# Optimization experiments

Hardware: AMD Instinct MI355X
Metric: run time of the kernel (lower is better)

## Reference

```python
import jax, jax.numpy as jnp
import numpy as np

N_HEAD = 16
EPS = 1e-5


def setup_inputs() -> dict:
    key = jax.random.key(0)
    ks = jax.random.split(key, 9)
    B, T, C = 2, 1024, 1024
    s = 0.02
    return {
        "x": jax.random.normal(ks[0], (B, T, C), jnp.float32),
        "Wq": jax.random.normal(ks[1], (C, C), jnp.float32) * s,
        "Wk": jax.random.normal(ks[2], (C, C), jnp.float32) * s,
        "Wv": jax.random.normal(ks[3], (C, C), jnp.float32) * s,
        "Wq2": jax.random.normal(ks[4], (C, C), jnp.float32) * s,
        "Wk2": jax.random.normal(ks[5], (C, C), jnp.float32) * s,
        "Wo": jax.random.normal(ks[6], (C, C), jnp.float32) * s,
        "mixture": jnp.full((1,), -5.0, jnp.float32),  # quartet_gate_init
        "quartet_scale": jnp.ones((1,), jnp.float32),
    }


def reference(x, Wq, Wk, Wv, Wq2, Wk2, Wo, mixture, quartet_scale):
    B, T, C = x.shape
    H = N_HEAD
    Dh = C // H
    scale = 1.0 / jnp.sqrt(jnp.asarray(Dh, x.dtype))

    def heads(W):
        # torch Linear: y = x @ W.T ; then view(B,T,H,Dh).transpose(1,2)
        return (x @ W.T).reshape(B, T, H, Dh).transpose(0, 2, 1, 3)  # [B,H,T,Dh]

    q, k, v = heads(Wq), heads(Wk), heads(Wv)
    q2, k2 = heads(Wq2), heads(Wk2)

    qk = jnp.einsum("bhqd,bhkd->bhqk", q, k) * scale      # [B,H,T,T]
    q2k2 = jnp.einsum("bhqd,bhkd->bhqk", q2, k2) * scale  # [B,H,T,T]

    def row_norm(s):
        mu = s.mean(axis=-1, keepdims=True)
        sigma = s.std(axis=-1, keepdims=True, ddof=1)  # torch std is unbiased
        return (s - mu) / (sigma + EPS)

    qk_n = row_norm(qk)
    q2k2_n = row_norm(q2k2)
    m = jax.nn.sigmoid(mixture)  # [1], broadcasts
    scores = (1.0 - m) * qk_n + m * (qk_n * q2k2_n) * quartet_scale

    causal = jnp.tril(jnp.ones((T, T), bool))  # [T,T]
    scores = jnp.where(causal, scores, -jnp.inf)
    attn = jax.nn.softmax(scores, axis=-1)  # [B,H,T,T]

    y = jnp.einsum("bhqk,bhkd->bhqd", attn, v)  # [B,H,T,Dh]
    y = y.transpose(0, 2, 1, 3).reshape(B, T, C)
    return y @ Wo.T
```

## Files before the change

kernel.cpp:

```cpp
#include <hip/hip_runtime.h>
#include <hip/hip_bf16.h>
#include <stdint.h>

#define TS 1024
#define CS 1024
#define NH 16
#define DHEAD 64
#define NBATCH 2
#define EPSV 1e-5f
#define MEG 1048576

typedef __bf16 bf16x8 __attribute__((ext_vector_type(8)));
typedef float  f32x4  __attribute__((ext_vector_type(4)));

#define MFMA(a, b, c) __builtin_amdgcn_mfma_f32_16x16x32_bf16((a), (b), (c), 0, 0, 0)

__device__ __forceinline__ float bf2f(ushort u){
  union { uint32_t i; float f; } v; v.i = ((uint32_t)u) << 16; return v.f;
}
__device__ __forceinline__ ushort f2bf(float f){
  union { float f; uint32_t i; } v; v.f = f;
  uint32_t r = v.i + 0x7FFFu + ((v.i >> 16) & 1u);
  return (ushort)(r >> 16);
}

__device__ __forceinline__ void gl_lds16(const ushort* g, ushort* l) {
  __builtin_amdgcn_global_load_lds(
      (const __attribute__((address_space(1))) void*)g,
      (__attribute__((address_space(3))) void*)l, 16, 0, 0);
}

__global__ __launch_bounds__(256)
void cast_all(const float* __restrict__ x,
              const float* __restrict__ Wq, const float* __restrict__ Wk,
              const float* __restrict__ Wv, const float* __restrict__ Wq2,
              const float* __restrict__ Wk2, const float* __restrict__ Wo,
              ushort* __restrict__ xb, ushort* __restrict__ wcat)
{
  const int XC = 524288, TOT = 2097152;
  for (int idx = blockIdx.x * 256 + threadIdx.x; idx < TOT; idx += 524288) {
    const float* s; ushort* d; int c;
    if (idx < XC) { s = x; d = xb; c = idx; }
    else {
      int r = idx - XC; int w = r >> 18; c = r & 262143;
      switch (w) {
        case 0:  s = Wq;  d = wcat;           break;
        case 1:  s = Wk;  d = wcat + 1*MEG;   break;
        case 2:  s = Wv;  d = wcat + 4*MEG;   break;
        case 3:  s = Wq2; d = wcat + 2*MEG;   break;
        case 4:  s = Wk2; d = wcat + 3*MEG;   break;
        default: s = Wo;  d = wcat + 5*MEG;   break;
      }
    }
    float4 v = *(const float4*)(s + (size_t)c * 4);
    ushort4 o; o.x = f2bf(v.x); o.y = f2bf(v.y); o.z = f2bf(v.z); o.w = f2bf(v.w);
    *(ushort4*)(d + (size_t)c * 4) = o;
  }
}

#define BN 128

__global__ __launch_bounds__(256, 2)
void gemm_proj(const ushort* __restrict__ A, const ushort* __restrict__ Bt,
               ushort* __restrict__ qb, ushort* __restrict__ kb,
               ushort* __restrict__ q2b, ushort* __restrict__ k2b,
               ushort* __restrict__ vtb,
               ushort* __restrict__ ktb, ushort* __restrict__ k2tb)
{
  __shared__ ushort a_s[64 * 64];
  __shared__ ushort b_s[128 * 64];

  const int bid = blockIdx.x;
  const int s   = (bid & 7) * 160 + (bid >> 3);
  const int n0  = (s >> 5) * BN;
  const int m0  = (s & 31) * 64;

  const int t  = threadIdx.x;
  const int w  = t >> 6, l = t & 63;
  const int wr = w >> 1, wc = w & 1;
  const int l15 = l & 15, l4 = l >> 4;
  const int r8 = l >> 3, g7 = l & 7;

  f32x4 acc[2][4] = {};

  for (int k0 = 0; k0 < CS; k0 += 64) {
    #pragma unroll
    for (int i = 0; i < 2; ++i) {
      int issue = w * 2 + i;
      int row   = issue * 8 + r8;
      int gs    = g7 ^ (row & 7);
      gl_lds16(&A[(size_t)(m0 + row) * CS + k0 + gs * 8], &a_s[issue * 512]);
    }
    #pragma unroll
    for (int i = 0; i < 4; ++i) {
      int issue = w * 4 + i;
      int row   = issue * 8 + r8;
      int gs    = g7 ^ (row & 7);
      gl_lds16(&Bt[(size_t)(n0 + row) * CS + k0 + gs * 8], &b_s[issue * 512]);
    }
    __syncthreads();

    #pragma unroll
    for (int ks = 0; ks < 2; ++ks) {
      bf16x8 af[2], bfr[4];
      #pragma unroll
      for (int mi = 0; mi < 2; ++mi) {
        int row = wr * 32 + mi * 16 + l15;
        int gl  = (ks * 4 + l4) ^ (row & 7);
        af[mi] = *(const bf16x8*)&a_s[row * 64 + gl * 8];
      }
      #pragma unroll
      for (int ni = 0; ni < 4; ++ni) {
        int row = wc * 64 + ni * 16 + l15;
        int gl  = (ks * 4 + l4) ^ (row & 7);
        bfr[ni] = *(const bf16x8*)&b_s[row * 64 + gl * 8];
      }
      #pragma unroll
      for (int mi = 0; mi < 2; ++mi)
        #pragma unroll
        for (int ni = 0; ni < 4; ++ni)
          acc[mi][ni] = MFMA(af[mi], bfr[ni], acc[mi][ni]);
    }

    __syncthreads();
  }

  #pragma unroll
  for (int mi = 0; mi < 2; ++mi) {
    #pragma unroll
    for (int ni = 0; ni < 4; ++ni) {
      int col  = n0 + wc * 64 + ni * 16 + l15;
      int row0 = m0 + wr * 32 + mi * 16 + l4 * 4;
      int seg  = col >> 10, cc = col & (CS - 1);
      if (seg < 4) {
        ushort* dst = (seg == 0) ? qb : (seg == 1) ? kb : (seg == 2) ? q2b : k2b;
        float sc = (seg & 1) ? 1.f : 0.125f;
        #pragma unroll
        for (int e = 0; e < 4; ++e)
          dst[(size_t)(row0 + e) * CS + cc] = f2bf(acc[mi][ni][e] * sc);
        if (seg == 1 || seg == 3) {
          int bb = row0 >> 10, tt = row0 & (TS - 1);
          int hh = cc >> 6, dd = cc & (DHEAD - 1);
          ushort* td = (seg == 1) ? ktb : k2tb;
          ushort4 o;
          o.x = f2bf(acc[mi][ni][0]); o.y = f2bf(acc[mi][ni][1]);
          o.z = f2bf(acc[mi][ni][2]); o.w = f2bf(acc[mi][ni][3]);
          *(ushort4*)&td[(((size_t)(bb * NH + hh) * DHEAD + dd) * TS) + tt] = o;
        }
      } else {
        int bb = row0 >> 10, tt = row0 & (TS - 1);
        int hh = cc >> 6, dd = cc & (DHEAD - 1);
        ushort4 o;
        o.x = f2bf(acc[mi][ni][0]); o.y = f2bf(acc[mi][ni][1]);
        o.z = f2bf(acc[mi][ni][2]); o.w = f2bf(acc[mi][ni][3]);
        *(ushort4*)&vtb[(((size_t)(bb * NH + hh) * DHEAD + dd) * TS) + tt] = o;
      }
    }
  }
}

__global__ __launch_bounds__(256, 2)
void gemm_out(const ushort* __restrict__ A, const ushort* __restrict__ Bt,
              float* __restrict__ C)
{
  __shared__ ushort a_s[64 * 32];
  __shared__ ushort b_s[64 * 32];

  const int bid = blockIdx.x;
  const int s   = (bid & 7) * 64 + (bid >> 3);
  const int n0  = (s >> 5) * 64;
  const int m0  = (s & 31) * 64;

  const int t  = threadIdx.x;
  const int w  = t >> 6, l = t & 63;
  const int wr = w >> 1, wc = w & 1;
  const int l15 = l & 15, l4 = l >> 4;
  const int rs = l >> 2;
  const int c8 = (l & 3) * 8;

  f32x4 acc[2][2] = {};

  for (int k0 = 0; k0 < CS; k0 += 32) {
    gl_lds16(&A [(size_t)(m0 + w * 16 + rs) * CS + k0 + c8], &a_s[w * 512]);
    gl_lds16(&Bt[(size_t)(n0 + w * 16 + rs) * CS + k0 + c8], &b_s[w * 512]);
    __syncthreads();

    bf16x8 af[2], bfr[2];
    #pragma unroll
    for (int mi = 0; mi < 2; ++mi)
      af[mi] = *(const bf16x8*)&a_s[(wr * 32 + mi * 16 + l15) * 32 + l4 * 8];
    #pragma unroll
    for (int ni = 0; ni < 2; ++ni)
      bfr[ni] = *(const bf16x8*)&b_s[(wc * 32 + ni * 16 + l15) * 32 + l4 * 8];

    #pragma unroll
    for (int mi = 0; mi < 2; ++mi)
      #pragma unroll
      for (int ni = 0; ni < 2; ++ni)
        acc[mi][ni] = MFMA(af[mi], bfr[ni], acc[mi][ni]);

    __syncthreads();
  }

  #pragma unroll
  for (int mi = 0; mi < 2; ++mi)
    #pragma unroll
    for (int ni = 0; ni < 2; ++ni)
      #pragma unroll
      for (int e = 0; e < 4; ++e)
        C[(size_t)(m0 + wr * 32 + mi * 16 + l4 * 4 + e) * CS +
          n0 + wc * 32 + ni * 16 + l15] = acc[mi][ni][e];
}

__global__ __launch_bounds__(256, 2)
void gram(const ushort* __restrict__ ktb, const ushort* __restrict__ k2tb,
          ushort* __restrict__ g1b, ushort* __restrict__ g2b,
          float* __restrict__ csb)
{
  __shared__ ushort t_s[64 * 128];

  const int mat = blockIdx.x & 1, z = blockIdx.x >> 1;
  const ushort* S = (mat ? k2tb : ktb) + (size_t)z * DHEAD * TS;

  const int t = threadIdx.x, w = t >> 6, l = t & 63;
  const int l15 = l & 15, l4 = l >> 4;

  f32x4 acc[4] = {};
  float csacc = 0.f;

  for (int tt = 0; tt < 8; ++tt) {
    const int t0 = tt * 128;
    __syncthreads();
    #pragma unroll
    for (int i = 0; i < 4; ++i) {
      int issue = w * 4 + i;
      int row = issue * 4 + l4;
      int gs  = l15 ^ (row & 15);
      gl_lds16(&S[(size_t)row * TS + t0 + gs * 8], &t_s[issue * 512]);
    }
    __syncthreads();

    {
      int r = w * 16 + l15;
      #pragma unroll
      for (int j = 0; j < 4; ++j) {
        int gg = ((l4 * 4 + j) ^ (r & 15)) * 8;
        uint4 vv = *(const uint4*)&t_s[r * 128 + gg];
        const ushort* pu = (const ushort*)&vv;
        #pragma unroll
        for (int e2 = 0; e2 < 8; ++e2) csacc += bf2f(pu[e2]);
      }
    }

    #pragma unroll
    for (int ks = 0; ks < 4; ++ks) {
      int ar = w * 16 + l15;
      bf16x8 af = *(const bf16x8*)&t_s[ar * 128 + ((ks * 4 + l4) ^ (ar & 15)) * 8];
      #pragma unroll
      for (int ni = 0; ni < 4; ++ni) {
        int br = ni * 16 + l15;
        bf16x8 bf_ = *(const bf16x8*)&t_s[br * 128 + ((ks * 4 + l4) ^ (br & 15)) * 8];
        acc[ni] = MFMA(af, bf_, acc[ni]);
      }
    }
  }

  csacc += __shfl_xor(csacc, 16);
  csacc += __shfl_xor(csacc, 32);
  if (l4 == 0)
    csb[(mat * 32 + z) * 64 + w * 16 + l15] = csacc;

  ushort* G = (mat ? g2b : g1b) + (size_t)z * 4096;
  #pragma unroll
  for (int ni = 0; ni < 4; ++ni)
    #pragma unroll
    for (int e = 0; e < 4; ++e)
      G[(w * 16 + l4 * 4 + e) * 64 + ni * 16 + l15] = f2bf(acc[ni][e]);
}

__global__ __launch_bounds__(256, 3)
void attn_fused(const ushort* __restrict__ qb, const ushort* __restrict__ kb,
                const ushort* __restrict__ q2b, const ushort* __restrict__ k2b,
                const ushort* __restrict__ vtb, ushort* __restrict__ yb,
                const ushort* __restrict__ g1b, const ushort* __restrict__ g2b,
                const float* __restrict__ csb,
                const float* __restrict__ mixture, const float* __restrict__ qsc)
{
  __shared__ ushort kbuf [2][4096];
  __shared__ ushort k2buf[2][4096];
  __shared__ ushort vbuf [2][4096];
  __shared__ ushort p_s  [2 * 32 * 40];

  const int idx  = blockIdx.x;
  const int pp   = idx >> 8;
  const int base = idx & 255;
  const int xcd  = base & 7;
  const int mm   = base >> 3;
  const int qq   = mm & 7;
  const int z    = (mm >> 3) * 8 + xcd;
  const int q32  = 31 - (pp * 8 + qq);
  const int b    = z >> 4, h = z & 15;
  const int m0   = q32 * 32;
  const int nkv  = (q32 >> 1) + 1;

  const ushort* Q  = qb  + (size_t)b * TS * CS + h * DHEAD;
  const ushort* Q2 = q2b + (size_t)b * TS * CS + h * DHEAD;
  const ushort* K  = kb  + (size_t)b * TS * CS + h * DHEAD;
  const ushort* K2 = k2b + (size_t)b * TS * CS + h * DHEAD;
  const ushort* Vt = vtb + (size_t)z * DHEAD * TS;
  const ushort* G1 = g1b + (size_t)z * 4096;
  const ushort* G2 = g2b + (size_t)z * 4096;
  ushort* Y = yb + (size_t)b * TS * CS + h * DHEAD;

  const int t = threadIdx.x, w = t >> 6, l = t & 63;
  const int l15 = l & 15, l4 = l >> 4;
  const int r8 = l >> 3, g7 = l & 7;
  const int p  = w >> 1, wr = w & 1;
  const int qrow = wr * 16 + l15;

  const float L2E = 1.44269504f;
  const float gm = 1.f / (1.f + __expf(-mixture[0]));
  const float mq2 = gm * qsc[0] * L2E;
  const float om2 = (1.f - gm) * L2E;

  auto stage_k = [&](int ti, int bs) {
    const int t0 = ti * 64;
    #pragma unroll
    for (int i = 0; i < 2; ++i) {
      int issue = w * 2 + i;
      int row = issue * 8 + r8;
      int gs  = g7 ^ (row & 7);
      gl_lds16(&K [(size_t)(t0 + row) * CS + gs * 8], &kbuf [bs][issue * 512]);
      gl_lds16(&K2[(size_t)(t0 + row) * CS + gs * 8], &k2buf[bs][issue * 512]);
    }
  };
  auto stage_v = [&](int ti, int bs) {
    const int t0 = ti * 64;
    #pragma unroll
    for (int i = 0; i < 2; ++i) {
      int issue = w * 2 + i;
      int row = issue * 8 + r8;
      int gs  = g7 ^ (row & 7);
      gl_lds16(&Vt[(size_t)row * TS + t0 + gs * 8], &vbuf[bs][issue * 512]);
    }
  };

  {
    int row = w * 8 + r8;
    int gs  = g7 ^ (row & 7);
    gl_lds16(&Q [(size_t)(m0 + row) * CS + gs * 8], &p_s[w * 512]);
    gl_lds16(&Q2[(size_t)(m0 + row) * CS + gs * 8], &kbuf[1][w * 512]);
  }
  stage_k(0, 0);
  stage_v(0, 0);
  __syncthreads();

  bf16x8 fq[2], fq2[2];
  #pragma unroll
  for (int ks = 0; ks < 2; ++ks) {
    int gg = ((ks * 4 + l4) ^ (qrow & 7)) * 8;
    fq [ks] = *(const bf16x8*)&p_s[qrow * 64 + gg];
    fq2[ks] = *(const bf16x8*)&kbuf[1][qrow * 64 + gg];
  }

  f32x4 U1[4] = {}, U2[4] = {};
  #pragma unroll
  for (int ks = 0; ks < 2; ++ks)
    #pragma unroll
    for (int ni = 0; ni < 4; ++ni) {
      bf16x8 bg = *(const bf16x8*)&G1[(ni * 16 + l15) * 64 + ks * 32 + l4 * 8];
      U1[ni] = MFMA(bg, fq[ks], U1[ni]);
    }
  #pragma unroll
  for (int ks = 0; ks < 2; ++ks)
    #pragma unroll
    for (int ni = 0; ni < 4; ++ni) {
      bf16x8 bg = *(const bf16x8*)&G2[(ni * 16 + l15) * 64 + ks * 32 + l4 * 8];
      U2[ni] = MFMA(bg, fq2[ks], U2[ni]);
    }

  float ssq1 = 0.f, md1 = 0.f, ssq2 = 0.f, md2 = 0.f;
  #pragma unroll
  for (int ni = 0; ni < 4; ++ni) {
    int gsq = (ni * 2 + (l4 >> 1)) ^ (qrow & 7);
    int off = qrow * 64 + gsq * 8 + (l4 & 1) * 4;
    ushort qa[4], qb2[4];
    *(uint2*)qa  = *(const uint2*)&p_s[off];
    *(uint2*)qb2 = *(const uint2*)&kbuf[1][off];
    float c1[4], c2[4];
    *(float4*)c1 = *(const float4*)&csb[z * 64 + ni * 16 + l4 * 4];
    *(float4*)c2 = *(const float4*)&csb[2048 + z * 64 + ni * 16 + l4 * 4];
    #pragma unroll
    for (int e = 0; e < 4; ++e) {
      float qv1 = bf2f(qa[e]), qv2 = bf2f(qb2[e]);
      ssq1 = fmaf(U1[ni][e], qv1, ssq1); md1 = fmaf(qv1, c1[e], md1);
      ssq2 = fmaf(U2[ni][e], qv2, ssq2); md2 = fmaf(qv2, c2[e], md2);
    }
  }
  ssq1 += __shfl_xor(ssq1, 16); md1 += __shfl_xor(md1, 16);
  ssq2 += __shfl_xor(ssq2, 16); md2 += __shfl_xor(md2, 16);
  ssq1 += __shfl_xor(ssq1, 32); md1 += __shfl_xor(md1, 32);
  ssq2 += __shfl_xor(ssq2, 32); md2 += __shfl_xor(md2, 32);

  const float mu1 = md1 * (1.f / TS), mu2 = md2 * (1.f / TS);
  const float va1 = (ssq1 - (float)TS * mu1 * mu1) * (1.f / (TS - 1));
  const float va2 = (ssq2 - (float)TS * mu2 * mu2) * (1.f / (TS - 1));
  const float iv1 = 1.f / (sqrtf(fmaxf(va1, 0.f)) + EPSV);
  const float iv2 = 1.f / (sqrtf(fmaxf(va2, 0.f)) + EPSV);
  __syncthreads();

  float lrow = 0.f;
  f32x4 accO[4] = {};

  for (int i = 0; i < nkv; ++i) {
    const int t0  = i * 64;
    const int cur = i & 1;
    if (i + 1 < nkv) { stage_k(i + 1, cur ^ 1); stage_v(i + 1, cur ^ 1); }

    const ushort* ks_ = kbuf [cur];
    const ushort* k2s_= k2buf[cur];

    f32x4 a1[2] = {}, a2[2] = {};
    #pragma unroll
    for (int ks = 0; ks < 2; ++ks) {
      bf16x8 bk[2], bk2[2];
      #pragma unroll
      for (int ni = 0; ni < 2; ++ni) {
        int j  = p * 32 + ni * 16 + l15;
        int gg = ((ks * 4 + l4) ^ (j & 7)) * 8;
        bk [ni] = *(const bf16x8*)&ks_ [j * 64 + gg];
        bk2[ni] = *(const bf16x8*)&k2s_[j * 64 + gg];
      }
      #pragma unroll
      for (int ni = 0; ni < 2; ++ni) {
        a1[ni] = MFMA(bk [ni], fq [ks], a1[ni]);
        a2[ni] = MFMA(bk2[ni], fq2[ks], a2[ni]);
      }
    }

    const int grow = m0 + qrow;
    #pragma unroll
    for (int ni = 0; ni < 2; ++ni) {
      float pe[4];
      #pragma unroll
      for (int e = 0; e < 4; ++e) {
        float n1 = (a1[ni][e] - mu1) * iv1;
        float n2 = (a2[ni][e] - mu2) * iv2;
        float sc = n1 * fmaf(mq2, n2, om2);
        float pv = exp2f(sc);
        int gcol = t0 + p * 32 + ni * 16 + l4 * 4 + e;
        pv = (gcol <= grow) ? pv : 0.f;
        lrow += pv;
        pe[e] = pv;
      }
      uint32_t pk01, pk23;
      asm("v_cvt_pk_bf16_f32 %0, %1, %2" : "=v"(pk01) : "v"(pe[0]), "v"(pe[1]));
      asm("v_cvt_pk_bf16_f32 %0, %1, %2" : "=v"(pk23) : "v"(pe[2]), "v"(pe[3]));
      uint2 pk; pk.x = pk01; pk.y = pk23;
      *(uint2*)&p_s[p * 1280 + qrow * 40 + ni * 16 + l4 * 4] = pk;
    }

    {
      bf16x8 ap = *(const bf16x8*)&p_s[p * 1280 + qrow * 40 + l4 * 8];
      #pragma unroll
      for (int ni = 0; ni < 4; ++ni) {
        int d  = ni * 16 + l15;
        int gg = ((p * 4 + l4) ^ (d & 7)) * 8;
        bf16x8 bv = *(const bf16x8*)&vbuf[cur][d * 64 + gg];
        accO[ni] = MFMA(ap, bv, accO[ni]);
      }
    }

    __syncthreads();
  }

  lrow += __shfl_xor(lrow, 16);
  lrow += __shfl_xor(lrow, 32);

  float* fb = (float*)kbuf;
  float* fl = (float*)k2buf;
  if (p == 1) {
    #pragma unroll
    for (int ni = 0; ni < 4; ++ni)
      #pragma unroll
      for (int e = 0; e < 4; ++e)
        fb[(wr * 16 + l4 * 4 + e) * 64 + ni * 16 + l15] = accO[ni][e];
    if (l4 == 0) fl[qrow] = lrow;
  }
  __syncthreads();
  if (p == 0) {
    float lt = lrow + fl[qrow];
    float il[4];
    #pragma unroll
    for (int e = 0; e < 4; ++e)
      il[e] = 1.f / __shfl(lt, l4 * 4 + e);
    #pragma unroll
    for (int ni = 0; ni < 4; ++ni)
      #pragma unroll
      for (int e = 0; e < 4; ++e) {
        float o = accO[ni][e] + fb[(wr * 16 + l4 * 4 + e) * 64 + ni * 16 + l15];
        Y[(size_t)(m0 + wr * 16 + l4 * 4 + e) * CS + ni * 16 + l15] = f2bf(o * il[e]);
      }
  }
}

extern "C" void kernel_launch(void* const* d_in, const int* in_sizes, int n_in,
                              void* d_out, int out_size, void* d_ws, size_t ws_size,
                              hipStream_t stream) {
  const float* x    = (const float*)d_in[0];
  const float* Wq   = (const float*)d_in[1];
  const float* Wk   = (const float*)d_in[2];
  const float* Wv   = (const float*)d_in[3];
  const float* Wq2  = (const float*)d_in[4];
  const float* Wk2  = (const float*)d_in[5];
  const float* Wo   = (const float*)d_in[6];
  const float* mixture = (const float*)d_in[7];
  const float* qsc  = (const float*)d_in[8];
  float* out = (float*)d_out;

  ushort* ws = (ushort*)d_ws;
  ushort* xb   = ws;
  ushort* wcat = xb   + (size_t)2 * MEG;
  ushort* qb   = wcat + (size_t)6 * MEG;
  ushort* q2b  = qb   + (size_t)2 * MEG;
  ushort* kb   = q2b  + (size_t)2 * MEG;
  ushort* k2b  = kb   + (size_t)2 * MEG;
  ushort* vtb  = k2b  + (size_t)2 * MEG;
  ushort* yb   = vtb  + (size_t)2 * MEG;
  ushort* ktb  = yb   + (size_t)2 * MEG;
  ushort* k2tb = ktb  + (size_t)2 * MEG;
  ushort* g1b  = k2tb + (size_t)2 * MEG;
  ushort* g2b  = g1b  + (size_t)(MEG / 8);
  float*  csb  = (float*)(g2b + (size_t)(MEG / 8));
  ushort* wob  = wcat + (size_t)5 * MEG;

  cast_all<<<2048, 256, 0, stream>>>(x, Wq, Wk, Wv, Wq2, Wk2, Wo, xb, wcat);

  gemm_proj<<<1280, 256, 0, stream>>>(
      xb, wcat, qb, kb, q2b, k2b, vtb, ktb, k2tb);

  gram<<<64, 256, 0, stream>>>(ktb, k2tb, g1b, g2b, csb);

  attn_fused<<<1024, 256, 0, stream>>>(qb, kb, q2b, k2b, vtb, yb,
                                       g1b, g2b, csb, mixture, qsc);

  gemm_out<<<512, 256, 0, stream>>>(yb, wob, out);
}
```

Baseline: 105.4 us.

## Double-buffer LDS in projection and output GEMMs and enlarge projection tile

Both GEMM kernels now keep two LDS buffers, so the next k-tile's global-to-LDS load is issued before the MFMAs on the current tile run. This overlaps memory latency with compute. The projection GEMM also grows its tile from 64x128 to 128x128 and switches to a plain 2D grid without the block-index swizzle, which raises operand reuse per block. The cost is twice the LDS per block (64KB for the projection kernel), a larger accumulator register footprint, and possibly worse L2 locality now that the swizzle is gone.

```diff
diff --git a/kernel.cpp b/kernel.cpp
--- a/kernel.cpp
+++ b/kernel.cpp
@@ -58,6 +58,7 @@
   }
 }
 
+#define BM 128
 #define BN 128
 
 __global__ __launch_bounds__(256, 2)
@@ -67,13 +68,11 @@
                ushort* __restrict__ vtb,
                ushort* __restrict__ ktb, ushort* __restrict__ k2tb)
 {
-  __shared__ ushort a_s[64 * 64];
-  __shared__ ushort b_s[128 * 64];
-
-  const int bid = blockIdx.x;
-  const int s   = (bid & 7) * 160 + (bid >> 3);
-  const int n0  = (s >> 5) * BN;
-  const int m0  = (s & 31) * 64;
+  __shared__ ushort a_s[2][BM * 64];
+  __shared__ ushort b_s[2][BN * 64];
+
+  const int n0 = blockIdx.x * BN;
+  const int m0 = blockIdx.y * BM;
 
   const int t  = threadIdx.x;
   const int w  = t >> 6, l = t & 63;
@@ -81,42 +80,44 @@
   const int l15 = l & 15, l4 = l >> 4;
   const int r8 = l >> 3, g7 = l & 7;
 
-  f32x4 acc[2][4] = {};
-
-  for (int k0 = 0; k0 < CS; k0 += 64) {
-    #pragma unroll
-    for (int i = 0; i < 2; ++i) {
-      int issue = w * 2 + i;
-      int row   = issue * 8 + r8;
-      int gs    = g7 ^ (row & 7);
-      gl_lds16(&A[(size_t)(m0 + row) * CS + k0 + gs * 8], &a_s[issue * 512]);
-    }
+  auto stage = [&](int kt, int bs) {
+    const int k0 = kt * 64;
     #pragma unroll
     for (int i = 0; i < 4; ++i) {
       int issue = w * 4 + i;
       int row   = issue * 8 + r8;
       int gs    = g7 ^ (row & 7);
-      gl_lds16(&Bt[(size_t)(n0 + row) * CS + k0 + gs * 8], &b_s[issue * 512]);
-    }
-    __syncthreads();
+      gl_lds16(&A [(size_t)(m0 + row) * CS + k0 + gs * 8], &a_s[bs][issue * 512]);
+      gl_lds16(&Bt[(size_t)(n0 + row) * CS + k0 + gs * 8], &b_s[bs][issue * 512]);
+    }
+  };
+
+  f32x4 acc[4][4] = {};
+
+  stage(0, 0);
+  __syncthreads();
+
+  for (int kt = 0; kt < 16; ++kt) {
+    const int cur = kt & 1;
+    if (kt < 15) stage(kt + 1, cur ^ 1);
 
     #pragma unroll
     for (int ks = 0; ks < 2; ++ks) {
-      bf16x8 af[2], bfr[4];
-      #pragma unroll
-      for (int mi = 0; mi < 2; ++mi) {
-        int row = wr * 32 + mi * 16 + l15;
+      bf16x8 af[4], bfr[4];
+      #pragma unroll
+      for (int mi = 0; mi < 4; ++mi) {
+        int row = wr * 64 + mi * 16 + l15;
         int gl  = (ks * 4 + l4) ^ (row & 7);
-        af[mi] = *(const bf16x8*)&a_s[row * 64 + gl * 8];
+        af[mi] = *(const bf16x8*)&a_s[cur][row * 64 + gl * 8];
       }
       #pragma unroll
       for (int ni = 0; ni < 4; ++ni) {
         int row = wc * 64 + ni * 16 + l15;
         int gl  = (ks * 4 + l4) ^ (row & 7);
-        bfr[ni] = *(const bf16x8*)&b_s[row * 64 + gl * 8];
-      }
-      #pragma unroll
-      for (int mi = 0; mi < 2; ++mi)
+        bfr[ni] = *(const bf16x8*)&b_s[cur][row * 64 + gl * 8];
+      }
+      #pragma unroll
+      for (int mi = 0; mi < 4; ++mi)
         #pragma unroll
         for (int ni = 0; ni < 4; ++ni)
           acc[mi][ni] = MFMA(af[mi], bfr[ni], acc[mi][ni]);
@@ -126,11 +127,11 @@
   }
 
   #pragma unroll
-  for (int mi = 0; mi < 2; ++mi) {
+  for (int mi = 0; mi < 4; ++mi) {
     #pragma unroll
     for (int ni = 0; ni < 4; ++ni) {
       int col  = n0 + wc * 64 + ni * 16 + l15;
-      int row0 = m0 + wr * 32 + mi * 16 + l4 * 4;
+      int row0 = m0 + wr * 64 + mi * 16 + l4 * 4;
       int seg  = col >> 10, cc = col & (CS - 1);
       if (seg < 4) {
         ushort* dst = (seg == 0) ? qb : (seg == 1) ? kb : (seg == 2) ? q2b : k2b;
@@ -163,8 +164,8 @@
 void gemm_out(const ushort* __restrict__ A, const ushort* __restrict__ Bt,
               float* __restrict__ C)
 {
-  __shared__ ushort a_s[64 * 32];
-  __shared__ ushort b_s[64 * 32];
+  __shared__ ushort a_s[2][64 * 32];
+  __shared__ ushort b_s[2][64 * 32];
 
   const int bid = blockIdx.x;
   const int s   = (bid & 7) * 64 + (bid >> 3);
@@ -178,20 +179,28 @@
   const int rs = l >> 2;
   const int c8 = (l & 3) * 8;
 
+  auto stage = [&](int kt, int bs) {
+    const int k0 = kt * 32;
+    gl_lds16(&A [(size_t)(m0 + w * 16 + rs) * CS + k0 + c8], &a_s[bs][w * 512]);
+    gl_lds16(&Bt[(size_t)(n0 + w * 16 + rs) * CS + k0 + c8], &b_s[bs][w * 512]);
+  };
+
   f32x4 acc[2][2] = {};
 
-  for (int k0 = 0; k0 < CS; k0 += 32) {
-    gl_lds16(&A [(size_t)(m0 + w * 16 + rs) * CS + k0 + c8], &a_s[w * 512]);
-    gl_lds16(&Bt[(size_t)(n0 + w * 16 + rs) * CS + k0 + c8], &b_s[w * 512]);
-    __syncthreads();
+  stage(0, 0);
+  __syncthreads();
+
+  for (int kt = 0; kt < 32; ++kt) {
+    const int cur = kt & 1;
+    if (kt < 31) stage(kt + 1, cur ^ 1);
 
     bf16x8 af[2], bfr[2];
     #pragma unroll
     for (int mi = 0; mi < 2; ++mi)
-      af[mi] = *(const bf16x8*)&a_s[(wr * 32 + mi * 16 + l15) * 32 + l4 * 8];
+      af[mi] = *(const bf16x8*)&a_s[cur][(wr * 32 + mi * 16 + l15) * 32 + l4 * 8];
     #pragma unroll
     for (int ni = 0; ni < 2; ++ni)
-      bfr[ni] = *(const bf16x8*)&b_s[(wc * 32 + ni * 16 + l15) * 32 + l4 * 8];
+      bfr[ni] = *(const bf16x8*)&b_s[cur][(wc * 32 + ni * 16 + l15) * 32 + l4 * 8];
 
     #pragma unroll
     for (int mi = 0; mi < 2; ++mi)
@@ -518,6 +527,7 @@
   const float* qsc  = (const float*)d_in[8];
   float* out = (float*)d_out;
 
+  const size_t MT = (size_t)NBATCH * TS;
   ushort* ws = (ushort*)d_ws;
   ushort* xb   = ws;
   ushort* wcat = xb   + (size_t)2 * MEG;
@@ -536,7 +546,7 @@
 
   cast_all<<<2048, 256, 0, stream>>>(x, Wq, Wk, Wv, Wq2, Wk2, Wo, xb, wcat);
 
-  gemm_proj<<<1280, 256, 0, stream>>>(
+  gemm_proj<<<dim3(5 * CS / BN, MT / BM, 1), 256, 0, stream>>>(
       xb, wcat, qb, kb, q2b, k2b, vtb, ktb, k2tb);
 
   gram<<<64, 256, 0, stream>>>(ktb, k2tb, g1b, g2b, csb);
```

Measured after the change: 115.5 us. +9.6%, slower.

## Deepen output GEMM K-tile with XOR-swizzled LDS and rebalance attention block order

Applied to the files above, without the earlier changes.

The output projection GEMM now stages 64-wide K slices per iteration instead of 32. The LDS layout uses an XOR swizzle of the 16-byte groups to avoid bank conflicts, which halves the number of barriers per K sweep. Separately, the attention kernel's mapping from block index to query tile is reordered so each dispatch wave mixes long and short causal tiles instead of strictly descending work. This trades a doubled LDS footprint in gemm_out for fewer syncs and better load balance across CUs.

```diff
diff --git a/kernel.cpp b/kernel.cpp
--- a/kernel.cpp
+++ b/kernel.cpp
@@ -163,8 +163,8 @@
 void gemm_out(const ushort* __restrict__ A, const ushort* __restrict__ Bt,
               float* __restrict__ C)
 {
-  __shared__ ushort a_s[64 * 32];
-  __shared__ ushort b_s[64 * 32];
+  __shared__ ushort a_s[64 * 64];
+  __shared__ ushort b_s[64 * 64];
 
   const int bid = blockIdx.x;
   const int s   = (bid & 7) * 64 + (bid >> 3);
@@ -175,29 +175,42 @@
   const int w  = t >> 6, l = t & 63;
   const int wr = w >> 1, wc = w & 1;
   const int l15 = l & 15, l4 = l >> 4;
-  const int rs = l >> 2;
-  const int c8 = (l & 3) * 8;
+  const int r8 = l >> 3, g7 = l & 7;
 
   f32x4 acc[2][2] = {};
 
-  for (int k0 = 0; k0 < CS; k0 += 32) {
-    gl_lds16(&A [(size_t)(m0 + w * 16 + rs) * CS + k0 + c8], &a_s[w * 512]);
-    gl_lds16(&Bt[(size_t)(n0 + w * 16 + rs) * CS + k0 + c8], &b_s[w * 512]);
-    __syncthreads();
-
-    bf16x8 af[2], bfr[2];
-    #pragma unroll
-    for (int mi = 0; mi < 2; ++mi)
-      af[mi] = *(const bf16x8*)&a_s[(wr * 32 + mi * 16 + l15) * 32 + l4 * 8];
-    #pragma unroll
-    for (int ni = 0; ni < 2; ++ni)
-      bfr[ni] = *(const bf16x8*)&b_s[(wc * 32 + ni * 16 + l15) * 32 + l4 * 8];
-
-    #pragma unroll
-    for (int mi = 0; mi < 2; ++mi)
-      #pragma unroll
-      for (int ni = 0; ni < 2; ++ni)
-        acc[mi][ni] = MFMA(af[mi], bfr[ni], acc[mi][ni]);
+  for (int k0 = 0; k0 < CS; k0 += 64) {
+    #pragma unroll
+    for (int i = 0; i < 2; ++i) {
+      int issue = w * 2 + i;
+      int row   = issue * 8 + r8;
+      int gs    = g7 ^ (row & 7);
+      gl_lds16(&A [(size_t)(m0 + row) * CS + k0 + gs * 8], &a_s[issue * 512]);
+      gl_lds16(&Bt[(size_t)(n0 + row) * CS + k0 + gs * 8], &b_s[issue * 512]);
+    }
+    __syncthreads();
+
+    #pragma unroll
+    for (int ks = 0; ks < 2; ++ks) {
+      bf16x8 af[2], bfr[2];
+      #pragma unroll
+      for (int mi = 0; mi < 2; ++mi) {
+        int row = wr * 32 + mi * 16 + l15;
+        int gl  = (ks * 4 + l4) ^ (row & 7);
+        af[mi] = *(const bf16x8*)&a_s[row * 64 + gl * 8];
+      }
+      #pragma unroll
+      for (int ni = 0; ni < 2; ++ni) {
+        int row = wc * 32 + ni * 16 + l15;
+        int gl  = (ks * 4 + l4) ^ (row & 7);
+        bfr[ni] = *(const bf16x8*)&b_s[row * 64 + gl * 8];
+      }
+      #pragma unroll
+      for (int mi = 0; mi < 2; ++mi)
+        #pragma unroll
+        for (int ni = 0; ni < 2; ++ni)
+          acc[mi][ni] = MFMA(af[mi], bfr[ni], acc[mi][ni]);
+    }
 
     __syncthreads();
   }
@@ -298,7 +311,8 @@
   const int mm   = base >> 3;
   const int qq   = mm & 7;
   const int z    = (mm >> 3) * 8 + xcd;
-  const int q32  = 31 - (pp * 8 + qq);
+  const int q32  = (pp == 0) ? (31 - qq) : (pp == 1) ? qq
+                 : (pp == 2) ? (23 - qq) : (8 + qq);
   const int b    = z >> 4, h = z & 15;
   const int m0   = q32 * 32;
   const int nkv  = (q32 >> 1) + 1;
```

Result: no change. 105.5 us (+0.1%).
